# Performance work log

Hardware: AMD Instinct MI355X
Metric: run time of the kernel (lower is better)

The kernel has to match this reference:

```python
import jax, jax.numpy as jnp
import numpy as np

N = 100000
E = 1600000
IN, HID, OUT = 128, 64, 32


def setup_inputs() -> dict:
    key = jax.random.key(0)
    ks = jax.random.split(key, 8)
    x = jax.random.normal(ks[0], (N, IN), dtype=jnp.float32)
    edge_index = jax.random.randint(ks[1], (2, E), 0, N, dtype=jnp.int32)
    eps = jax.random.normal(ks[2], (N, OUT), dtype=jnp.float32)
    W1 = jax.random.normal(ks[3], (IN, HID), dtype=jnp.float32) / np.sqrt(IN)
    b1 = jnp.zeros((HID,), jnp.float32)
    Wmu = jax.random.normal(ks[4], (HID, OUT), dtype=jnp.float32) / np.sqrt(HID)
    bmu = jnp.zeros((OUT,), jnp.float32)
    Wls = jax.random.normal(ks[5], (HID, OUT), dtype=jnp.float32) / np.sqrt(HID)
    bls = jnp.zeros((OUT,), jnp.float32)
    return dict(x=x, edge_index=edge_index, eps=eps, W1=W1, b1=b1,
                Wmu=Wmu, bmu=bmu, Wls=Wls, bls=bls)


def reference(x, edge_index, eps, W1, b1, Wmu, bmu, Wls, bls):
    n = x.shape[0]
    src, dst = edge_index[0], edge_index[1]
    # GCN with self-loops and symmetric normalization (PyG GCNConv default)
    loop = jnp.arange(n, dtype=src.dtype)
    s = jnp.concatenate([src, loop])   # [E+N]
    d = jnp.concatenate([dst, loop])
    deg = jax.ops.segment_sum(jnp.ones_like(s, jnp.float32), d, num_segments=n)
    dis = jax.lax.rsqrt(jnp.maximum(deg, 1.0))  # deg >= 1 due to self-loops
    norm = dis[s] * dis[d]                       # [E+N]

    def gcn_conv(h, W, b):
        h = h @ W                                # transform first (small dim)
        msg = h[s] * norm[:, None]               # gather over edges
        return jax.ops.segment_sum(msg, d, num_segments=n) + b

    h = jax.nn.relu(gcn_conv(x, W1, b1))
    # F.normalize(h, p=2, dim=-1)
    h = h / jnp.maximum(jnp.linalg.norm(h, axis=-1, keepdims=True), 1e-12)
    mu = gcn_conv(h, Wmu, bmu)
    logstd = gcn_conv(h, Wls, bls)
    # reparametrize (training mode): mu + randn * exp(clamp(logstd, -10, 10))
    z = mu + eps * jnp.exp(jnp.clip(logstd, -10.0, 10.0))
    # decode: sigmoid(<z_i, z_j>) over original edges
    adj_pred = jax.nn.sigmoid(jnp.sum(z[src] * z[dst], axis=1))
    return adj_pred, mu, logstd
```

## Files before the change

### kernel.cpp

```cpp
#include <hip/hip_runtime.h>
#include <hip/hip_fp16.h>

#define NN 100000
#define NE 1600000
#define W_BKT 128
#define NB_BKT ((NN + W_BKT - 1) / W_BKT)
#define TILE_E 16384
#define NT ((NE + TILE_E - 1) / TILE_E)
#define STAGE_CAP 4352

typedef _Float16 half2v __attribute__((ext_vector_type(2)));
typedef _Float16 half8v __attribute__((ext_vector_type(8)));
typedef float float2v __attribute__((ext_vector_type(2)));


__global__ __launch_bounds__(256) void k_cnt(const int* __restrict__ dst,
                                             int* __restrict__ counts) {
    __shared__ int hc[NB_BKT];
    int tid = threadIdx.x;
    for (int i = tid; i < NB_BKT; i += 256) hc[i] = 0;
    __syncthreads();
    int base = blockIdx.x * TILE_E;
    int lim = base + TILE_E; if (lim > NE) lim = NE;
    for (int e = base + tid; e < lim; e += 256)
        atomicAdd(&hc[dst[e] >> 7], 1);
    __syncthreads();
    for (int i = tid; i < NB_BKT; i += 256)
        counts[blockIdx.x * NB_BKT + i] = hc[i];
}

__global__ __launch_bounds__(1024) void k_bscan(const int* __restrict__ counts,
                                                int* __restrict__ bucket_base) {
    __shared__ int buf[1024];
    int tid = threadIdx.x;
    int total = 0;
    if (tid < NB_BKT)
        for (int t = 0; t < NT; ++t) total += counts[t * NB_BKT + tid];
    buf[tid] = total;
    __syncthreads();
    for (int off = 1; off < 1024; off <<= 1) {
        int v = (tid >= off) ? buf[tid - off] : 0;
        __syncthreads();
        buf[tid] += v;
        __syncthreads();
    }
    if (tid < NB_BKT) bucket_base[tid] = buf[tid] - total;
    if (tid == 0) bucket_base[NB_BKT] = NE;
}

__global__ __launch_bounds__(256) void k_offs(const int* __restrict__ bucket_base,
                                              int* __restrict__ counts) {
    int b = blockIdx.x * 256 + threadIdx.x;
    if (b >= NB_BKT) return;
    int off = bucket_base[b];
    for (int t = 0; t < NT; ++t) {
        int c = counts[t * NB_BKT + b];
        counts[t * NB_BKT + b] = off;
        off += c;
    }
}

__global__ __launch_bounds__(256) void k_place(const int* __restrict__ src,
                                               const int* __restrict__ dst,
                                               const int* __restrict__ counts,
                                               int* __restrict__ ebuf) {
    __shared__ int cur[NB_BKT];
    int tid = threadIdx.x;
    for (int i = tid; i < NB_BKT; i += 256)
        cur[i] = counts[blockIdx.x * NB_BKT + i];
    __syncthreads();
    int base = blockIdx.x * TILE_E;
    int lim = base + TILE_E; if (lim > NE) lim = NE;
    for (int e = base + tid; e < lim; e += 256) {
        int s = src[e], d = dst[e];
        int pos = atomicAdd(&cur[d >> 7], 1);
        ebuf[pos] = (s << 7) | (d & 127);
    }
}

__global__ __launch_bounds__(256) void k_build(const int* __restrict__ bucket_base,
                                               const int* __restrict__ ebuf,
                                               int* __restrict__ csr_src,
                                               int* __restrict__ row_ptr,
                                               float* __restrict__ dis) {
    __shared__ int deg[W_BKT];
    __shared__ int pre[W_BKT];
    __shared__ int cur[W_BKT];
    __shared__ int stage[STAGE_CAP];
    int b = blockIdx.x;
    int tid = threadIdx.x;
    int beg = bucket_base[b], end = bucket_base[b + 1];
    int n = end - beg;
    if (tid < W_BKT) deg[tid] = 0;
    __syncthreads();
    bool fits = (n <= STAGE_CAP);
    if (fits) {
        for (int i = tid; i < n; i += 256) {
            int val = ebuf[beg + i];
            stage[i] = val;
            atomicAdd(&deg[val & 127], 1);
        }
    } else {
        for (int i = tid; i < n; i += 256)
            atomicAdd(&deg[ebuf[beg + i] & 127], 1);
    }
    __syncthreads();
    if (tid < W_BKT) pre[tid] = deg[tid];
    __syncthreads();
    for (int off = 1; off < W_BKT; off <<= 1) {
        int v = (tid >= off && tid < W_BKT) ? pre[tid - off] : 0;
        __syncthreads();
        if (tid < W_BKT) pre[tid] += v;
        __syncthreads();
    }
    if (tid < W_BKT) {
        int v = b * W_BKT + tid;
        int rp = beg + pre[tid] - deg[tid];
        if (v < NN) {
            row_ptr[v] = rp;
            dis[v] = rsqrtf((float)(1 + deg[tid]));
        }
        cur[tid] = rp;
    }
    if (b == NB_BKT - 1 && tid == 0) row_ptr[NN] = NE;
    __syncthreads();
    if (fits) {
        for (int i = tid; i < n; i += 256) {
            int val = stage[i];
            int pos = atomicAdd(&cur[val & 127], 1);
            csr_src[pos] = val >> 7;
        }
    } else {
        for (int i = tid; i < n; i += 256) {
            int val = ebuf[beg + i];
            int pos = atomicAdd(&cur[val & 127], 1);
            csr_src[pos] = val >> 7;
        }
    }
}


__global__ __launch_bounds__(256) void k_gemm1(const float* __restrict__ x,
                                               const float* __restrict__ W1,
                                               const float* __restrict__ dis,
                                               _Float16* __restrict__ t1) {
    __shared__ float Wl[128 * 64];
    __shared__ float Xl[16 * 128];
    int tid = threadIdx.x;
    const float4* W4 = (const float4*)W1;
    float4* Wl4 = (float4*)Wl;
    for (int i = tid; i < 128 * 16; i += 256) Wl4[i] = W4[i];
    long rowbase = (long)blockIdx.x * 16;
    const float4* X4 = (const float4*)(x + rowbase * 128);
    float4* Xl4 = (float4*)Xl;
    for (int i = tid; i < 16 * 32; i += 256) Xl4[i] = X4[i];
    __syncthreads();
    int col = tid & 63, rg = tid >> 6;
    float acc[4] = {0.f, 0.f, 0.f, 0.f};
    for (int k = 0; k < 128; ++k) {
        float w = Wl[k * 64 + col];
#pragma unroll
        for (int i = 0; i < 4; ++i) acc[i] += Xl[(rg * 4 + i) * 128 + k] * w;
    }
#pragma unroll
    for (int i = 0; i < 4; ++i) {
        long row = rowbase + rg * 4 + i;
        t1[row * 64 + col] = (_Float16)(acc[i] * dis[row]);
    }
}

__global__ __launch_bounds__(256) void k_gemm2(const float* __restrict__ h,
                                               const float* __restrict__ Wmu,
                                               const float* __restrict__ Wls,
                                               const float* __restrict__ dis,
                                               _Float16* __restrict__ t2) {
    __shared__ float Wl[64 * 64];
    __shared__ float Hl[16 * 64];
    int tid = threadIdx.x;
    for (int i = tid; i < 64 * 64; i += 256) {
        int k = i >> 6, j = i & 63;
        Wl[i] = (j < 32) ? Wmu[k * 32 + j] : Wls[k * 32 + j - 32];
    }
    long rowbase = (long)blockIdx.x * 16;
    const float4* H4 = (const float4*)(h + rowbase * 64);
    float4* Hl4 = (float4*)Hl;
    for (int i = tid; i < 16 * 16; i += 256) Hl4[i] = H4[i];
    __syncthreads();
    int col = tid & 63, rg = tid >> 6;
    float acc[4] = {0.f, 0.f, 0.f, 0.f};
    for (int k = 0; k < 64; ++k) {
        float w = Wl[k * 64 + col];
#pragma unroll
        for (int i = 0; i < 4; ++i) acc[i] += Hl[(rg * 4 + i) * 64 + k] * w;
    }
#pragma unroll
    for (int i = 0; i < 4; ++i) {
        long row = rowbase + rg * 4 + i;
        t2[row * 64 + col] = (_Float16)(acc[i] * dis[row]);
    }
}


__global__ __launch_bounds__(256) void k_agg1(const half2v* __restrict__ tv,
                                              const int* __restrict__ row_ptr,
                                              const int* __restrict__ csr_src,
                                              const float* __restrict__ dis,
                                              const float* __restrict__ b1,
                                              float* __restrict__ h) {
    int lane = threadIdx.x & 63;
    int j2 = lane & 31;
    int v = blockIdx.x * 8 + (threadIdx.x >> 6) * 2 + (lane >> 5);
    int beg = row_ptr[v], end = row_ptr[v + 1];
    float acc0 = 0.f, acc1 = 0.f;
    for (int base = beg; base < end; base += 32) {
        int cnt = end - base; if (cnt > 32) cnt = 32;
        int idx = 0;
        if (j2 < cnt) idx = csr_src[base + j2];
        int k = 0;
        for (; k + 8 <= cnt; k += 8) {
            int s0 = __shfl(idx, k, 32),     s1 = __shfl(idx, k + 1, 32),
                s2 = __shfl(idx, k + 2, 32), s3 = __shfl(idx, k + 3, 32),
                s4 = __shfl(idx, k + 4, 32), s5 = __shfl(idx, k + 5, 32),
                s6 = __shfl(idx, k + 6, 32), s7 = __shfl(idx, k + 7, 32);
            half2v r0 = tv[s0 * 32 + j2];
            half2v r1 = tv[s1 * 32 + j2];
            half2v r2 = tv[s2 * 32 + j2];
            half2v r3 = tv[s3 * 32 + j2];
            half2v r4 = tv[s4 * 32 + j2];
            half2v r5 = tv[s5 * 32 + j2];
            half2v r6 = tv[s6 * 32 + j2];
            half2v r7 = tv[s7 * 32 + j2];
            acc0 += (float)r0.x; acc1 += (float)r0.y;
            acc0 += (float)r1.x; acc1 += (float)r1.y;
            acc0 += (float)r2.x; acc1 += (float)r2.y;
            acc0 += (float)r3.x; acc1 += (float)r3.y;
            acc0 += (float)r4.x; acc1 += (float)r4.y;
            acc0 += (float)r5.x; acc1 += (float)r5.y;
            acc0 += (float)r6.x; acc1 += (float)r6.y;
            acc0 += (float)r7.x; acc1 += (float)r7.y;
        }
        for (; k < cnt; ++k) {
            int s = __shfl(idx, k, 32);
            half2v r = tv[s * 32 + j2];
            acc0 += (float)r.x; acc1 += (float)r.y;
        }
    }
    float dv = dis[v];
    half2v rv = tv[v * 32 + j2];
    float val0 = dv * (acc0 + (float)rv.x) + b1[2 * j2];
    float val1 = dv * (acc1 + (float)rv.y) + b1[2 * j2 + 1];
    val0 = fmaxf(val0, 0.0f);
    val1 = fmaxf(val1, 0.0f);
    float ss = val0 * val0 + val1 * val1;
#pragma unroll
    for (int m = 1; m < 32; m <<= 1) ss += __shfl_xor(ss, m);
    float scale = 1.0f / fmaxf(sqrtf(ss), 1e-12f);
    float2v* h2 = (float2v*)h;
    float2v hv; hv.x = val0 * scale; hv.y = val1 * scale;
    h2[v * 32 + j2] = hv;
}

__global__ __launch_bounds__(256) void k_agg2(const half2v* __restrict__ tv,
                                              const int* __restrict__ row_ptr,
                                              const int* __restrict__ csr_src,
                                              const float* __restrict__ dis,
                                              const float* __restrict__ bmu,
                                              const float* __restrict__ bls,
                                              const float* __restrict__ eps,
                                              float* __restrict__ mu,
                                              float* __restrict__ ls,
                                              _Float16* __restrict__ zh) {
    int lane = threadIdx.x & 63;
    int j2 = lane & 31;
    int v = blockIdx.x * 8 + (threadIdx.x >> 6) * 2 + (lane >> 5);
    int beg = row_ptr[v], end = row_ptr[v + 1];
    float acc0 = 0.f, acc1 = 0.f;
    for (int base = beg; base < end; base += 32) {
        int cnt = end - base; if (cnt > 32) cnt = 32;
        int idx = 0;
        if (j2 < cnt) idx = csr_src[base + j2];
        int k = 0;
        for (; k + 8 <= cnt; k += 8) {
            int s0 = __shfl(idx, k, 32),     s1 = __shfl(idx, k + 1, 32),
                s2 = __shfl(idx, k + 2, 32), s3 = __shfl(idx, k + 3, 32),
                s4 = __shfl(idx, k + 4, 32), s5 = __shfl(idx, k + 5, 32),
                s6 = __shfl(idx, k + 6, 32), s7 = __shfl(idx, k + 7, 32);
            half2v r0 = tv[s0 * 32 + j2];
            half2v r1 = tv[s1 * 32 + j2];
            half2v r2 = tv[s2 * 32 + j2];
            half2v r3 = tv[s3 * 32 + j2];
            half2v r4 = tv[s4 * 32 + j2];
            half2v r5 = tv[s5 * 32 + j2];
            half2v r6 = tv[s6 * 32 + j2];
            half2v r7 = tv[s7 * 32 + j2];
            acc0 += (float)r0.x; acc1 += (float)r0.y;
            acc0 += (float)r1.x; acc1 += (float)r1.y;
            acc0 += (float)r2.x; acc1 += (float)r2.y;
            acc0 += (float)r3.x; acc1 += (float)r3.y;
            acc0 += (float)r4.x; acc1 += (float)r4.y;
            acc0 += (float)r5.x; acc1 += (float)r5.y;
            acc0 += (float)r6.x; acc1 += (float)r6.y;
            acc0 += (float)r7.x; acc1 += (float)r7.y;
        }
        for (; k < cnt; ++k) {
            int s = __shfl(idx, k, 32);
            half2v r = tv[s * 32 + j2];
            acc0 += (float)r.x; acc1 += (float)r.y;
        }
    }
    float dv = dis[v];
    half2v rv = tv[v * 32 + j2];
    float bb0 = (j2 < 16) ? bmu[2 * j2]     : bls[2 * j2 - 32];
    float bb1 = (j2 < 16) ? bmu[2 * j2 + 1] : bls[2 * j2 - 31];
    float val0 = dv * (acc0 + (float)rv.x) + bb0;
    float val1 = dv * (acc1 + (float)rv.y) + bb1;
    float o0 = __shfl_xor(val0, 16);
    float o1 = __shfl_xor(val1, 16);
    float2v* mu2 = (float2v*)mu;
    float2v* ls2 = (float2v*)ls;
    half2v* z2  = (half2v*)zh;
    const float2* e2 = (const float2*)eps;
    if (j2 < 16) {
        float2v mv; mv.x = val0; mv.y = val1;
        __builtin_nontemporal_store(mv, &mu2[v * 16 + j2]);
        float2 ev = e2[v * 16 + j2];
        float l0 = fminf(fmaxf(o0, -10.0f), 10.0f);
        float l1 = fminf(fmaxf(o1, -10.0f), 10.0f);
        half2v zw;
        zw.x = (_Float16)(val0 + ev.x * expf(l0));
        zw.y = (_Float16)(val1 + ev.y * expf(l1));
        z2[v * 16 + j2] = zw;
    } else {
        float2v lv; lv.x = val0; lv.y = val1;
        __builtin_nontemporal_store(lv, &ls2[v * 16 + (j2 - 16)]);
    }
}

__global__ __launch_bounds__(256) void k_decode(const _Float16* __restrict__ zh,
                                                const int* __restrict__ src,
                                                const int* __restrict__ dst,
                                                float* __restrict__ out) {
    long t = (long)blockIdx.x * 256 + threadIdx.x;
    long e = t >> 2; int l = (int)(t & 3);
    if (e >= NE) return;
    int s = src[e], d = dst[e];
    const half8v* z8 = (const half8v*)zh;
    half8v a = z8[s * 4 + l];
    half8v b = z8[d * 4 + l];
    float p = 0.f;
#pragma unroll
    for (int i = 0; i < 8; ++i) p += (float)a[i] * (float)b[i];
    p += __shfl_xor(p, 1);
    p += __shfl_xor(p, 2);
    if (l == 0) out[e] = 1.0f / (1.0f + expf(-p));
}

extern "C" void kernel_launch(void* const* d_in, const int* in_sizes, int n_in,
                              void* d_out, int out_size, void* d_ws, size_t ws_size,
                              hipStream_t stream) {
    const float* x   = (const float*)d_in[0];
    const int*   ei  = (const int*)d_in[1];
    const float* eps = (const float*)d_in[2];
    const float* W1  = (const float*)d_in[3];
    const float* b1  = (const float*)d_in[4];
    const float* Wmu = (const float*)d_in[5];
    const float* bmu = (const float*)d_in[6];
    const float* Wls = (const float*)d_in[7];
    const float* bls = (const float*)d_in[8];
    const int* src = ei;
    const int* dst = ei + NE;

    float* out = (float*)d_out;
    float* adj = out;
    float* mu  = out + NE;
    float* ls  = mu + (long)NN * 32;

    float* dis      = (float*)d_ws;
    int*   row_ptr  = (int*)(dis + NN);
    int*   bucket_base = row_ptr + 100004;
    int*   counts   = bucket_base + 784;
    int*   ebuf     = counts + 76640;
    int*   csr_src  = ebuf + NE;
    _Float16* t     = (_Float16*)(csr_src + NE);
    float* h        = (float*)(t + (long)NN * 64);
    _Float16* zh    = (_Float16*)(h + (long)NN * 64 + 12);

    const int B = 256;

    k_cnt  <<<NT, B, 0, stream>>>(dst, counts);
    k_bscan<<<1, 1024, 0, stream>>>(counts, bucket_base);
    k_offs <<<(NB_BKT + B - 1) / B, B, 0, stream>>>(bucket_base, counts);
    k_place<<<NT, B, 0, stream>>>(src, dst, counts, ebuf);
    k_build<<<NB_BKT, B, 0, stream>>>(bucket_base, ebuf, csr_src, row_ptr, dis);

    k_gemm1<<<NN / 16, B, 0, stream>>>(x, W1, dis, t);
    k_agg1 <<<NN / 8, B, 0, stream>>>((const half2v*)t, row_ptr, csr_src, dis, b1, h);

    k_gemm2<<<NN / 16, B, 0, stream>>>(h, Wmu, Wls, dis, t);
    k_agg2 <<<NN / 8, B, 0, stream>>>((const half2v*)t, row_ptr, csr_src, dis,
                                      bmu, bls, eps, mu, ls, zh);

    k_decode<<<(int)(((long)NE * 4 + B - 1) / B), B, 0, stream>>>(zh, src, dst, adj);
}
```

Before: 394.5 us.

## Use split-fp16 MFMA for both dense transforms with prepacked weight fragments

Replaces the shared-memory FP32 scalar GEMMs with MFMA 16x16x32 fp16 instructions, emulating fp32 accuracy by splitting each operand into hi and lo halves and issuing three MFMAs per tile. A new one-block kernel prepacks W1 and the concatenated Wmu/Wls into per-lane fragment layouts, stored in the reused counts workspace. This removes the per-block weight staging into LDS and the scalar FMA loop, at the cost of extra split arithmetic, one extra launch, and a small loss of precision against true fp32.

```diff
diff --git a/kernel.cpp b/kernel.cpp
--- a/kernel.cpp
+++ b/kernel.cpp
@@ -12,6 +12,7 @@
 typedef _Float16 half2v __attribute__((ext_vector_type(2)));
 typedef _Float16 half8v __attribute__((ext_vector_type(8)));
 typedef float float2v __attribute__((ext_vector_type(2)));
+typedef float float4v __attribute__((ext_vector_type(4)));
 
 
 __global__ __launch_bounds__(256) void k_cnt(const int* __restrict__ dst,
@@ -140,63 +141,139 @@
 }
 
 
+__global__ __launch_bounds__(256) void k_wprep(const float* __restrict__ W1,
+                                               const float* __restrict__ Wmu,
+                                               const float* __restrict__ Wls,
+                                               _Float16* __restrict__ wf1h,
+                                               _Float16* __restrict__ wf1l,
+                                               _Float16* __restrict__ wf2h,
+                                               _Float16* __restrict__ wf2l) {
+    int tid = threadIdx.x;
+    for (int f = tid; f < 4 * 4 * 64; f += 256) {
+        int lane = f & 63;
+        int kc = (f >> 6) & 3;
+        int ct = f >> 8;
+        int col = ct * 16 + (lane & 15);
+        int k0 = kc * 32 + (lane >> 4) * 8;
+#pragma unroll
+        for (int j = 0; j < 8; ++j) {
+            float w = W1[(k0 + j) * 64 + col];
+            _Float16 hi = (_Float16)w;
+            wf1h[f * 8 + j] = hi;
+            wf1l[f * 8 + j] = (_Float16)(w - (float)hi);
+        }
+    }
+    for (int f = tid; f < 4 * 2 * 64; f += 256) {
+        int lane = f & 63;
+        int kc = (f >> 6) & 1;
+        int ct = f >> 7;
+        int col = ct * 16 + (lane & 15);
+        int k0 = kc * 32 + (lane >> 4) * 8;
+#pragma unroll
+        for (int j = 0; j < 8; ++j) {
+            int k = k0 + j;
+            float w = (col < 32) ? Wmu[k * 32 + col] : Wls[k * 32 + (col - 32)];
+            _Float16 hi = (_Float16)w;
+            wf2h[f * 8 + j] = hi;
+            wf2l[f * 8 + j] = (_Float16)(w - (float)hi);
+        }
+    }
+}
+
+__device__ __forceinline__ void split8(const float4 a, const float4 b,
+                                       half8v& hi, half8v& lo) {
+    float v[8] = {a.x, a.y, a.z, a.w, b.x, b.y, b.z, b.w};
+#pragma unroll
+    for (int i = 0; i < 8; ++i) {
+        _Float16 h = (_Float16)v[i];
+        hi[i] = h;
+        lo[i] = (_Float16)(v[i] - (float)h);
+    }
+}
+
 __global__ __launch_bounds__(256) void k_gemm1(const float* __restrict__ x,
-                                               const float* __restrict__ W1,
+                                               const _Float16* __restrict__ wf1h,
+                                               const _Float16* __restrict__ wf1l,
                                                const float* __restrict__ dis,
                                                _Float16* __restrict__ t1) {
-    __shared__ float Wl[128 * 64];
-    __shared__ float Xl[16 * 128];
-    int tid = threadIdx.x;
-    const float4* W4 = (const float4*)W1;
-    float4* Wl4 = (float4*)Wl;
-    for (int i = tid; i < 128 * 16; i += 256) Wl4[i] = W4[i];
-    long rowbase = (long)blockIdx.x * 16;
-    const float4* X4 = (const float4*)(x + rowbase * 128);
-    float4* Xl4 = (float4*)Xl;
-    for (int i = tid; i < 16 * 32; i += 256) Xl4[i] = X4[i];
-    __syncthreads();
-    int col = tid & 63, rg = tid >> 6;
-    float acc[4] = {0.f, 0.f, 0.f, 0.f};
-    for (int k = 0; k < 128; ++k) {
-        float w = Wl[k * 64 + col];
-#pragma unroll
-        for (int i = 0; i < 4; ++i) acc[i] += Xl[(rg * 4 + i) * 128 + k] * w;
-    }
-#pragma unroll
-    for (int i = 0; i < 4; ++i) {
-        long row = rowbase + rg * 4 + i;
-        t1[row * 64 + col] = (_Float16)(acc[i] * dis[row]);
+    int tid = threadIdx.x;
+    int lane = tid & 63;
+    int wv = tid >> 6;
+    int wrow = blockIdx.x * 64 + wv * 16;
+    int cl = lane & 15, kg = lane >> 4;
+    const half8v* Bh = (const half8v*)wf1h;
+    const half8v* Bl = (const half8v*)wf1l;
+    float4v acc[4] = {};
+    int r = wrow + cl;
+    long rr = (r < NN) ? r : (NN - 1);
+    const float4* xp = (const float4*)(x + rr * 128);
+#pragma unroll
+    for (int kc = 0; kc < 4; ++kc) {
+        float4 xa = xp[kc * 8 + kg * 2];
+        float4 xb = xp[kc * 8 + kg * 2 + 1];
+        half8v ah, al;
+        split8(xa, xb, ah, al);
+#pragma unroll
+        for (int ct = 0; ct < 4; ++ct) {
+            half8v bh = Bh[(ct * 4 + kc) * 64 + lane];
+            half8v bl = Bl[(ct * 4 + kc) * 64 + lane];
+            acc[ct] = __builtin_amdgcn_mfma_f32_16x16x32_f16(ah, bh, acc[ct], 0, 0, 0);
+            acc[ct] = __builtin_amdgcn_mfma_f32_16x16x32_f16(al, bh, acc[ct], 0, 0, 0);
+            acc[ct] = __builtin_amdgcn_mfma_f32_16x16x32_f16(ah, bl, acc[ct], 0, 0, 0);
+        }
+    }
+#pragma unroll
+    for (int j = 0; j < 4; ++j) {
+        int row = wrow + kg * 4 + j;
+        if (row < NN) {
+            float dv = dis[row];
+#pragma unroll
+            for (int ct = 0; ct < 4; ++ct)
+                t1[(long)row * 64 + ct * 16 + cl] = (_Float16)(acc[ct][j] * dv);
+        }
     }
 }
 
 __global__ __launch_bounds__(256) void k_gemm2(const float* __restrict__ h,
-                                               const float* __restrict__ Wmu,
-                                               const float* __restrict__ Wls,
+                                               const _Float16* __restrict__ wf2h,
+                                               const _Float16* __restrict__ wf2l,
                                                const float* __restrict__ dis,
                                                _Float16* __restrict__ t2) {
-    __shared__ float Wl[64 * 64];
-    __shared__ float Hl[16 * 64];
-    int tid = threadIdx.x;
-    for (int i = tid; i < 64 * 64; i += 256) {
-        int k = i >> 6, j = i & 63;
-        Wl[i] = (j < 32) ? Wmu[k * 32 + j] : Wls[k * 32 + j - 32];
-    }
-    long rowbase = (long)blockIdx.x * 16;
-    const float4* H4 = (const float4*)(h + rowbase * 64);
-    float4* Hl4 = (float4*)Hl;
-    for (int i = tid; i < 16 * 16; i += 256) Hl4[i] = H4[i];
-    __syncthreads();
-    int col = tid & 63, rg = tid >> 6;
-    float acc[4] = {0.f, 0.f, 0.f, 0.f};
-    for (int k = 0; k < 64; ++k) {
-        float w = Wl[k * 64 + col];
-#pragma unroll
-        for (int i = 0; i < 4; ++i) acc[i] += Hl[(rg * 4 + i) * 64 + k] * w;
-    }
-#pragma unroll
-    for (int i = 0; i < 4; ++i) {
-        long row = rowbase + rg * 4 + i;
-        t2[row * 64 + col] = (_Float16)(acc[i] * dis[row]);
+    int tid = threadIdx.x;
+    int lane = tid & 63;
+    int wv = tid >> 6;
+    int wrow = blockIdx.x * 64 + wv * 16;
+    int cl = lane & 15, kg = lane >> 4;
+    const half8v* Bh = (const half8v*)wf2h;
+    const half8v* Bl = (const half8v*)wf2l;
+    float4v acc[4] = {};
+    int r = wrow + cl;
+    long rr = (r < NN) ? r : (NN - 1);
+    const float4* hp = (const float4*)(h + rr * 64);
+#pragma unroll
+    for (int kc = 0; kc < 2; ++kc) {
+        float4 xa = hp[kc * 8 + kg * 2];
+        float4 xb = hp[kc * 8 + kg * 2 + 1];
+        half8v ah, al;
+        split8(xa, xb, ah, al);
+#pragma unroll
+        for (int ct = 0; ct < 4; ++ct) {
+            half8v bh = Bh[(ct * 2 + kc) * 64 + lane];
+            half8v bl = Bl[(ct * 2 + kc) * 64 + lane];
+            acc[ct] = __builtin_amdgcn_mfma_f32_16x16x32_f16(ah, bh, acc[ct], 0, 0, 0);
+            acc[ct] = __builtin_amdgcn_mfma_f32_16x16x32_f16(al, bh, acc[ct], 0, 0, 0);
+            acc[ct] = __builtin_amdgcn_mfma_f32_16x16x32_f16(ah, bl, acc[ct], 0, 0, 0);
+        }
+    }
+#pragma unroll
+    for (int j = 0; j < 4; ++j) {
+        int row = wrow + kg * 4 + j;
+        if (row < NN) {
+            float dv = dis[row];
+#pragma unroll
+            for (int ct = 0; ct < 4; ++ct)
+                t2[(long)row * 64 + ct * 16 + cl] = (_Float16)(acc[ct][j] * dv);
+        }
     }
 }
 
@@ -385,18 +462,24 @@
     float* h        = (float*)(t + (long)NN * 64);
     _Float16* zh    = (_Float16*)(h + (long)NN * 64 + 12);
 
+    _Float16* wf1h = (_Float16*)counts;
+    _Float16* wf1l = wf1h + 8192;
+    _Float16* wf2h = wf1l + 8192;
+    _Float16* wf2l = wf2h + 4096;
+
     const int B = 256;
 
     k_cnt  <<<NT, B, 0, stream>>>(dst, counts);
     k_bscan<<<1, 1024, 0, stream>>>(counts, bucket_base);
     k_offs <<<(NB_BKT + B - 1) / B, B, 0, stream>>>(bucket_base, counts);
     k_place<<<NT, B, 0, stream>>>(src, dst, counts, ebuf);
+    k_wprep<<<1, B, 0, stream>>>(W1, Wmu, Wls, wf1h, wf1l, wf2h, wf2l);
     k_build<<<NB_BKT, B, 0, stream>>>(bucket_base, ebuf, csr_src, row_ptr, dis);
 
-    k_gemm1<<<NN / 16, B, 0, stream>>>(x, W1, dis, t);
+    k_gemm1<<<(NN + 63) / 64, B, 0, stream>>>(x, wf1h, wf1l, dis, t);
     k_agg1 <<<NN / 8, B, 0, stream>>>((const half2v*)t, row_ptr, csr_src, dis, b1, h);
 
-    k_gemm2<<<NN / 16, B, 0, stream>>>(h, Wmu, Wls, dis, t);
+    k_gemm2<<<(NN + 63) / 64, B, 0, stream>>>(h, wf2h, wf2l, dis, t);
     k_agg2 <<<NN / 8, B, 0, stream>>>((const half2v*)t, row_ptr, csr_src, dis,
                                       bmu, bls, eps, mu, ls, zh);
 
```

New measurement: 362.9 us. 8.0% less time.
